# Optimization experiments

Hardware: AMD Instinct MI355X
Metric: run time of the kernel (lower is better)

## Reference

```python
import jax, jax.numpy as jnp
import numpy as np

H = 64      # hidden_dim
NH = 4      # attention heads
HD = H // NH
NC = 13     # num_classes
NF = 8      # node features


def setup_inputs() -> dict:
    key = jax.random.key(0)
    ks = iter(jax.random.split(key, 32))
    B, T, N, E = 4, 16, 4096, 32768
    s = 0.05
    d = {}
    d["node_features"] = jax.random.normal(next(ks), (B, T, N, NF), jnp.float32)
    d["edge_index"] = jax.random.randint(next(ks), (T, 2, E), 0, N, jnp.int32)
    # spatial conv (Linear(NF,H), ReLU, Linear(H,H))
    d["sc_w1"] = jax.random.normal(next(ks), (H, NF), jnp.float32) * s
    d["sc_b1"] = jnp.zeros((H,), jnp.float32)
    d["sc_w2"] = jax.random.normal(next(ks), (H, H), jnp.float32) * s
    d["sc_b2"] = jnp.zeros((H,), jnp.float32)
    # 2-layer LSTM (pytorch gate order i,f,g,o)
    for l in range(2):
        d[f"lstm_w_ih{l}"] = jax.random.normal(next(ks), (4 * H, H), jnp.float32) * s
        d[f"lstm_w_hh{l}"] = jax.random.normal(next(ks), (4 * H, H), jnp.float32) * s
        d[f"lstm_b_ih{l}"] = jnp.zeros((4 * H,), jnp.float32)
        d[f"lstm_b_hh{l}"] = jnp.zeros((4 * H,), jnp.float32)
    # MultiheadAttention in_proj / out_proj
    d["attn_w_in"] = jax.random.normal(next(ks), (3 * H, H), jnp.float32) * s
    d["attn_b_in"] = jnp.zeros((3 * H,), jnp.float32)
    d["attn_w_out"] = jax.random.normal(next(ks), (H, H), jnp.float32) * s
    d["attn_b_out"] = jnp.zeros((H,), jnp.float32)
    # predictor MLP (dropout inactive at eval)
    d["p_w1"] = jax.random.normal(next(ks), (2 * H, H), jnp.float32) * s
    d["p_b1"] = jnp.zeros((2 * H,), jnp.float32)
    d["p_w2"] = jax.random.normal(next(ks), (H, 2 * H), jnp.float32) * s
    d["p_b2"] = jnp.zeros((H,), jnp.float32)
    d["p_w3"] = jax.random.normal(next(ks), (NC, H), jnp.float32) * s
    d["p_b3"] = jnp.zeros((NC,), jnp.float32)
    return d


def _lstm_layer(x, w_ih, w_hh, b_ih, b_hh):
    # x: (T, BN, H_in) -> (T, BN, H)
    BN = x.shape[1]
    Hh = w_hh.shape[1]

    def step(carry, xt):
        h, c = carry
        z = xt @ w_ih.T + h @ w_hh.T + (b_ih + b_hh)
        i, f, g, o = jnp.split(z, 4, axis=-1)
        c = jax.nn.sigmoid(f) * c + jax.nn.sigmoid(i) * jnp.tanh(g)
        h = jax.nn.sigmoid(o) * jnp.tanh(c)
        return (h, c), h

    h0 = jnp.zeros((BN, Hh), x.dtype)
    _, ys = jax.lax.scan(step, (h0, h0), x)
    return ys


def _forward(node_features, edge_index, sc_w1, sc_b1, sc_w2, sc_b2,
             lstm_w_ih0, lstm_w_hh0, lstm_b_ih0, lstm_b_hh0,
             lstm_w_ih1, lstm_w_hh1, lstm_b_ih1, lstm_b_hh1,
             attn_w_in, attn_b_in, attn_w_out, attn_b_out,
             p_w1, p_b1, p_w2, p_b2, p_w3, p_b3):
    B, T, N, _ = node_features.shape
    # spatial conv applied to every (b,t,n)
    h = jax.nn.relu(jnp.einsum('btnf,hf->btnh', node_features, sc_w1) + sc_b1)
    h = jnp.einsum('btnh,gh->btng', h, sc_w2) + sc_b2  # (B,T,N,H)

    def agg_step(_, inp):
        h_t, edges = inp  # (B,N,H), (2,E)
        src, dst = edges[0], edges[1]
        msgs = h_t[:, src]  # (B,E,H) gathered from pre-update h_t (matches torch)
        ssum = jax.vmap(lambda m: jax.ops.segment_sum(m, dst, num_segments=N))(msgs)
        cnt = jax.ops.segment_sum(jnp.ones(dst.shape, h_t.dtype), dst, num_segments=N)
        mean = ssum / jnp.maximum(cnt, 1.0)[None, :, None]
        h_new = jnp.where(cnt[None, :, None] > 0, (h_t + mean) * 0.5, h_t)
        return None, h_new

    _, h_agg = jax.lax.scan(agg_step, None, (h.transpose(1, 0, 2, 3), edge_index))
    h = h_agg.transpose(1, 0, 2, 3)  # (B,T,N,H)

    # per-node temporal sequence: (T, B*N, H)
    x = h.transpose(0, 2, 1, 3).reshape(B * N, T, H).transpose(1, 0, 2)
    x = _lstm_layer(x, lstm_w_ih0, lstm_w_hh0, lstm_b_ih0, lstm_b_hh0)
    x = _lstm_layer(x, lstm_w_ih1, lstm_w_hh1, lstm_b_ih1, lstm_b_hh1)
    x = x.transpose(1, 0, 2)  # (BN,T,H)

    # multi-head self-attention (batch_first)
    qkv = x @ attn_w_in.T + attn_b_in
    q, k, v = jnp.split(qkv, 3, axis=-1)
    BN = q.shape[0]
    q = q.reshape(BN, T, NH, HD)
    k = k.reshape(BN, T, NH, HD)
    v = v.reshape(BN, T, NH, HD)
    scores = jnp.einsum('bthd,bshd->bhts', q, k) / jnp.sqrt(jnp.float32(HD)).astype(x.dtype)
    attn = jax.nn.softmax(scores, axis=-1)
    o = jnp.einsum('bhts,bshd->bthd', attn, v).reshape(BN, T, H)
    o = o @ attn_w_out.T + attn_b_out

    final = o[:, -1, :]  # (BN,H)
    z = jax.nn.relu(final @ p_w1.T + p_b1)
    z = jax.nn.relu(z @ p_w2.T + p_b2)
    logits = z @ p_w3.T + p_b3
    return logits.reshape(B, N, NC)


def reference(node_features, edge_index, sc_w1, sc_b1, sc_w2, sc_b2,
              lstm_w_ih0, lstm_w_hh0, lstm_b_ih0, lstm_b_hh0,
              lstm_w_ih1, lstm_w_hh1, lstm_b_ih1, lstm_b_hh1,
              attn_w_in, attn_b_in, attn_w_out, attn_b_out,
              p_w1, p_b1, p_w2, p_b2, p_w3, p_b3):
    return _forward(node_features, edge_index, sc_w1, sc_b1, sc_w2, sc_b2,
                    lstm_w_ih0, lstm_w_hh0, lstm_b_ih0, lstm_b_hh0,
                    lstm_w_ih1, lstm_w_hh1, lstm_b_ih1, lstm_b_hh1,
                    attn_w_in, attn_b_in, attn_w_out, attn_b_out,
                    p_w1, p_b1, p_w2, p_b2, p_w3, p_b3)
```

## Files before the change

kernel.cpp:

```cpp
#include <hip/hip_runtime.h>

constexpr int kB  = 4;
constexpr int kT  = 16;
constexpr int kN  = 4096;
constexpr int kBN = kB * kN;
constexpr int kE  = 32768;
constexpr int kNC = 13;

typedef _Float16 f16x8 __attribute__((ext_vector_type(8)));
typedef _Float16 f16x4 __attribute__((ext_vector_type(4)));
typedef float f32x4 __attribute__((ext_vector_type(4)));

__device__ __forceinline__ float sigm(float x) { return 1.f / (1.f + __expf(-x)); }
__device__ __forceinline__ float tanh_(float x) {
  float e = __expf(2.f * x);
  return 1.f - 2.f / (e + 1.f);
}

__device__ __forceinline__ void barrier_lds() {
  asm volatile("s_waitcnt lgkmcnt(0)\n\ts_barrier" ::: "memory");
}

__device__ __forceinline__ f32x4 mm3(f16x8 ah, f16x8 al, f16x8 bh, f16x8 bl, f32x4 acc) {
  acc = __builtin_amdgcn_mfma_f32_16x16x32_f16(ah, bh, acc, 0, 0, 0);
  acc = __builtin_amdgcn_mfma_f32_16x16x32_f16(ah, bl, acc, 0, 0, 0);
  acc = __builtin_amdgcn_mfma_f32_16x16x32_f16(al, bh, acc, 0, 0, 0);
  return acc;
}

__device__ __forceinline__ void split8(const float* p, f16x8& hi, f16x8& lo) {
  float4 u0 = *(const float4*)p, u1 = *(const float4*)(p + 4);
  float vv[8] = {u0.x, u0.y, u0.z, u0.w, u1.x, u1.y, u1.z, u1.w};
#pragma unroll
  for (int j = 0; j < 8; ++j) {
    _Float16 hj = (_Float16)vv[j];
    hi[j] = hj;
    lo[j] = (_Float16)(vv[j] - (float)hj);
  }
}

__device__ __forceinline__ void split8T(const float* base, int kbase, int seq,
                                        f16x8& hi, f16x8& lo) {
  float vv[8];
#pragma unroll
  for (int j = 0; j < 8; ++j) vv[j] = base[(kbase + j) * 68 + seq];
#pragma unroll
  for (int j = 0; j < 8; ++j) {
    _Float16 hj = (_Float16)vv[j];
    hi[j] = hj;
    lo[j] = (_Float16)(vv[j] - (float)hj);
  }
}

__device__ __forceinline__ unsigned int packf(float v) {
  _Float16 h = (_Float16)v;
  _Float16 l = (_Float16)(v - (float)h);
  unsigned short uh = __builtin_bit_cast(unsigned short, h);
  unsigned short ul = __builtin_bit_cast(unsigned short, l);
  return (unsigned int)uh | ((unsigned int)ul << 16);
}
__device__ __forceinline__ float up2(unsigned int w) {
  _Float16 h = __builtin_bit_cast(_Float16, (unsigned short)(w & 0xFFFFu));
  _Float16 l = __builtin_bit_cast(_Float16, (unsigned short)(w >> 16));
  return (float)h + (float)l;
}
__device__ __forceinline__ void unpack8(const unsigned int* w, f16x8& hi, f16x8& lo) {
#pragma unroll
  for (int j = 0; j < 8; ++j) {
    hi[j] = __builtin_bit_cast(_Float16, (unsigned short)(w[j] & 0xFFFFu));
    lo[j] = __builtin_bit_cast(_Float16, (unsigned short)(w[j] >> 16));
  }
}

__global__ __launch_bounds__(256, 2) void conv_kernel(
    const float* __restrict__ nf, const float* __restrict__ w1,
    const float* __restrict__ b1, const float* __restrict__ w2,
    const float* __restrict__ b2, unsigned int* __restrict__ hpk) {
  __shared__ unsigned int act[256 * 68];
  int tid = threadIdx.x;
  int w = tid >> 6, lane = tid & 63;
  int q = lane >> 4, i = lane & 15;
  int flat0 = blockIdx.x * 256;
  int bb = flat0 >> 16;
  int t = (flat0 >> 12) & 15;
  int n0 = flat0 & 4095;

  f16x8 w1h[4], w1l[4];
  f16x8 w2h[4][2], w2l[4][2];
  float bias1[4], bias2[4];
#pragma unroll
  for (int nt = 0; nt < 4; ++nt) {
    int n = nt * 16 + i;
    if (q == 0) split8(w1 + n * 8, w1h[nt], w1l[nt]);
    else { w1h[nt] = (f16x8)0; w1l[nt] = (f16x8)0; }
#pragma unroll
    for (int ks = 0; ks < 2; ++ks)
      split8(w2 + n * 64 + ks * 32 + q * 8, w2h[nt][ks], w2l[nt][ks]);
    bias1[nt] = b1[n];
    bias2[nt] = b2[n];
  }

  f16x8 xh[4], xl[4];
#pragma unroll
  for (int Mt = 0; Mt < 4; ++Mt) {
    if (q == 0)
      split8(nf + (size_t)(flat0 + w * 64 + Mt * 16 + i) * 8, xh[Mt], xl[Mt]);
    else { xh[Mt] = (f16x8)0; xl[Mt] = (f16x8)0; }
  }
#pragma unroll
  for (int Mt = 0; Mt < 4; ++Mt)
#pragma unroll
    for (int nt = 0; nt < 4; ++nt) {
      f32x4 acc = {bias1[nt], bias1[nt], bias1[nt], bias1[nt]};
      acc = mm3(xh[Mt], xl[Mt], w1h[nt], w1l[nt], acc);
#pragma unroll
      for (int r = 0; r < 4; ++r)
        act[(w * 64 + Mt * 16 + q * 4 + r) * 68 + nt * 16 + i] =
            packf(fmaxf(acc[r], 0.f));
    }
  __syncthreads();

  f32x4 acc2[4][4];
#pragma unroll
  for (int Mt = 0; Mt < 4; ++Mt)
#pragma unroll
    for (int nt = 0; nt < 4; ++nt) {
      acc2[Mt][nt][0] = bias2[nt]; acc2[Mt][nt][1] = bias2[nt];
      acc2[Mt][nt][2] = bias2[nt]; acc2[Mt][nt][3] = bias2[nt];
    }
#pragma unroll
  for (int ks = 0; ks < 2; ++ks)
#pragma unroll
    for (int Mt = 0; Mt < 4; ++Mt) {
      const unsigned int* p = &act[(w * 64 + Mt * 16 + i) * 68 + ks * 32 + q * 8];
      unsigned int wd[8];
#pragma unroll
      for (int j = 0; j < 4; ++j) {
        uint2 u = *(const uint2*)(p + j * 2);
        wd[2 * j] = u.x; wd[2 * j + 1] = u.y;
      }
      f16x8 ah, al;
      unpack8(wd, ah, al);
#pragma unroll
      for (int nt = 0; nt < 4; ++nt)
        acc2[Mt][nt] = mm3(ah, al, w2h[nt][ks], w2l[nt][ks], acc2[Mt][nt]);
    }
  __syncthreads();
#pragma unroll
  for (int Mt = 0; Mt < 4; ++Mt)
#pragma unroll
    for (int nt = 0; nt < 4; ++nt)
#pragma unroll
      for (int r = 0; r < 4; ++r)
        act[(w * 64 + Mt * 16 + q * 4 + r) * 68 + nt * 16 + i] =
            packf(acc2[Mt][nt][r]);
  __syncthreads();
  size_t tbase = ((size_t)t * kBN + (size_t)bb * kN + n0) * 64;
#pragma unroll
  for (int k = 0; k < 16; ++k) {
    int d0 = (k * 256 + tid) * 4;
    int node = d0 >> 6, ch = d0 & 63;
    uint2 a = *(const uint2*)&act[node * 68 + ch];
    uint2 b = *(const uint2*)&act[node * 68 + ch + 2];
    uint4 vv = {a.x, a.y, b.x, b.y};
    *(uint4*)(hpk + tbase + d0) = vv;
  }
}

__global__ __launch_bounds__(256) void count_kernel(
    const int* __restrict__ ei, int* __restrict__ cnt) {
  int i = blockIdx.x * 256 + threadIdx.x;
  int t = i >> 15, e = i & (kE - 1);
  int dst = ei[t * 2 * kE + kE + e];
  atomicAdd(&cnt[t * kN + dst], 1);
}

__global__ __launch_bounds__(1024) void scan_kernel(
    const int* __restrict__ cnt, int* __restrict__ off, int* __restrict__ cur) {
  __shared__ int sdata[1024];
  int t = blockIdx.x;
  int tid = threadIdx.x;
  const int* c = cnt + t * kN;
  int v0 = c[tid * 4], v1 = c[tid * 4 + 1], v2 = c[tid * 4 + 2], v3 = c[tid * 4 + 3];
  int s = v0 + v1 + v2 + v3;
  sdata[tid] = s;
  __syncthreads();
  for (int d = 1; d < 1024; d <<= 1) {
    int add = (tid >= d) ? sdata[tid - d] : 0;
    __syncthreads();
    sdata[tid] += add;
    __syncthreads();
  }
  int base = sdata[tid] - s;
  int o = t * kN + tid * 4;
  off[o] = base;            cur[o] = base;
  off[o + 1] = base + v0;   cur[o + 1] = base + v0;
  off[o + 2] = base + v0 + v1;        cur[o + 2] = base + v0 + v1;
  off[o + 3] = base + v0 + v1 + v2;   cur[o + 3] = base + v0 + v1 + v2;
}

__global__ __launch_bounds__(256) void place_kernel(
    const int* __restrict__ ei, int* __restrict__ cur, int* __restrict__ csr) {
  int i = blockIdx.x * 256 + threadIdx.x;
  int t = i >> 15, e = i & (kE - 1);
  int src = ei[t * 2 * kE + e];
  int dst = ei[t * 2 * kE + kE + e];
  int pos = atomicAdd(&cur[t * kN + dst], 1);
  csr[t * kE + pos] = src;
}

__global__ __launch_bounds__(256) void gather_kernel(
    const unsigned int* __restrict__ hpk, const int* __restrict__ csr,
    const int* __restrict__ off, const int* __restrict__ cnt,
    _Float16* __restrict__ xhi, _Float16* __restrict__ xlo) {
  int blk = blockIdx.x;
  int t = (blk & 7) | ((blk >> 13) << 3);
  int idx = (blk >> 3) & 1023;
  int d = idx * 4 + (threadIdx.x >> 6);
  int lane = threadIdx.x & 63;
  int b = lane >> 4, cq = lane & 15;
  int o = off[t * kN + d];
  int c = cnt[t * kN + d];
  size_t tb = ((size_t)t * kBN + (size_t)b * kN) * 64 + cq * 4;
  const int* cs = csr + t * kE + o;
  float s[4] = {0.f, 0.f, 0.f, 0.f};
  int j = 0;
  for (; j + 4 <= c; j += 4) {
    int i0 = cs[j], i1 = cs[j + 1], i2 = cs[j + 2], i3 = cs[j + 3];
    uint4 v0 = *(const uint4*)(hpk + tb + (size_t)i0 * 64);
    uint4 v1 = *(const uint4*)(hpk + tb + (size_t)i1 * 64);
    uint4 v2 = *(const uint4*)(hpk + tb + (size_t)i2 * 64);
    uint4 v3 = *(const uint4*)(hpk + tb + (size_t)i3 * 64);
    s[0] += up2(v0.x) + up2(v1.x) + up2(v2.x) + up2(v3.x);
    s[1] += up2(v0.y) + up2(v1.y) + up2(v2.y) + up2(v3.y);
    s[2] += up2(v0.z) + up2(v1.z) + up2(v2.z) + up2(v3.z);
    s[3] += up2(v0.w) + up2(v1.w) + up2(v2.w) + up2(v3.w);
  }
  for (; j < c; ++j) {
    int i0 = cs[j];
    uint4 v0 = *(const uint4*)(hpk + tb + (size_t)i0 * 64);
    s[0] += up2(v0.x); s[1] += up2(v0.y); s[2] += up2(v0.z); s[3] += up2(v0.w);
  }
  uint4 hv = *(const uint4*)(hpk + tb + (size_t)d * 64);
  float hvf[4] = {up2(hv.x), up2(hv.y), up2(hv.z), up2(hv.w)};
  f16x4 ohi, olo;
  float inv = (c > 0) ? 1.f / (float)c : 0.f;
#pragma unroll
  for (int u = 0; u < 4; ++u) {
    float ov = (c > 0) ? (hvf[u] + s[u] * inv) * 0.5f : hvf[u];
    _Float16 hi = (_Float16)ov;
    ohi[u] = hi;
    olo[u] = (_Float16)(ov - (float)hi);
  }
  *(f16x4*)(xhi + tb + (size_t)d * 64) = ohi;
  *(f16x4*)(xlo + tb + (size_t)d * 64) = olo;
}

__global__ __launch_bounds__(512, 2) void lstm2_kernel(
    const _Float16* __restrict__ xhi, const _Float16* __restrict__ xlo,
    _Float16* __restrict__ yhi, _Float16* __restrict__ ylo,
    const float* __restrict__ wih0, const float* __restrict__ whh0,
    const float* __restrict__ bih0, const float* __restrict__ bhh0,
    const float* __restrict__ wih1, const float* __restrict__ whh1,
    const float* __restrict__ bih1, const float* __restrict__ bhh1) {
  __shared__ _Float16 h1f[2][4][2][2][512];
  __shared__ _Float16 h2f[2][4][2][2][512];
  int tid = threadIdx.x;
  int grp = tid >> 8;
  int cb = (tid >> 6) & 3, lane = tid & 63;
  int q = lane >> 4, i = lane & 15;
  int s0 = blockIdx.x * 64;

  const float* Wih = grp ? wih1 : wih0;
  const float* Whh = grp ? whh1 : whh0;
  const float* Bih = grp ? bih1 : bih0;
  const float* Bhh = grp ? bhh1 : bhh0;

  f16x8 wr[2][4][2][2];
#pragma unroll
  for (int mat = 0; mat < 2; ++mat) {
    const float* W = mat ? Whh : Wih;
#pragma unroll
    for (int g = 0; g < 4; ++g) {
      int row = (g * 4 + cb) * 16 + i;
#pragma unroll
      for (int ks = 0; ks < 2; ++ks)
        split8(W + row * 64 + ks * 32 + q * 8, wr[mat][g][ks][0], wr[mat][g][ks][1]);
    }
  }
  int ch = cb * 16 + i;
  float bias4[4];
#pragma unroll
  for (int g = 0; g < 4; ++g) bias4[g] = Bih[g * 64 + ch] + Bhh[g * 64 + ch];
  float cst[4][4];
#pragma unroll
  for (int Mt = 0; Mt < 4; ++Mt)
#pragma unroll
    for (int r = 0; r < 4; ++r) cst[Mt][r] = 0.f;
  int ks2 = ch >> 5, q2 = (ch >> 3) & 3, j2 = ch & 7;
  int p = 0;

  for (int it = 0; it < kT + 1; ++it) {
    if (grp == 0) {
      if (it < kT) {
        int t = it;
#pragma unroll
        for (int mp = 0; mp < 2; ++mp) {
          f32x4 acc[2][4];
#pragma unroll
          for (int ml = 0; ml < 2; ++ml)
#pragma unroll
            for (int g = 0; g < 4; ++g) {
              acc[ml][g][0] = bias4[g]; acc[ml][g][1] = bias4[g];
              acc[ml][g][2] = bias4[g]; acc[ml][g][3] = bias4[g];
            }
#pragma unroll
          for (int ks = 0; ks < 2; ++ks) {
            f16x8 xah[2], xal[2];
#pragma unroll
            for (int ml = 0; ml < 2; ++ml) {
              size_t base = ((size_t)t * kBN + s0 + (2 * mp + ml) * 16 + i) * 64 + ks * 32 + q * 8;
              xah[ml] = *(const f16x8*)(xhi + base);
              xal[ml] = *(const f16x8*)(xlo + base);
            }
#pragma unroll
            for (int g = 0; g < 4; ++g)
#pragma unroll
              for (int ml = 0; ml < 2; ++ml)
                acc[ml][g] = mm3(xah[ml], xal[ml], wr[0][g][ks][0], wr[0][g][ks][1], acc[ml][g]);
          }
          if (t > 0) {
#pragma unroll
            for (int ks = 0; ks < 2; ++ks) {
              f16x8 hah[2], hal[2];
#pragma unroll
              for (int ml = 0; ml < 2; ++ml) {
                hah[ml] = *(const f16x8*)&h1f[p][2 * mp + ml][ks][0][lane * 8];
                hal[ml] = *(const f16x8*)&h1f[p][2 * mp + ml][ks][1][lane * 8];
              }
#pragma unroll
              for (int g = 0; g < 4; ++g)
#pragma unroll
                for (int ml = 0; ml < 2; ++ml)
                  acc[ml][g] = mm3(hah[ml], hal[ml], wr[1][g][ks][0], wr[1][g][ks][1], acc[ml][g]);
            }
          }
#pragma unroll
          for (int ml = 0; ml < 2; ++ml) {
            int Mt = 2 * mp + ml;
#pragma unroll
            for (int r = 0; r < 4; ++r) {
              float zi = acc[ml][0][r], zf = acc[ml][1][r];
              float zg = acc[ml][2][r], zo = acc[ml][3][r];
              float ig = sigm(zi), fg = sigm(zf), gg = tanh_(zg), og = sigm(zo);
              float c = fg * cst[Mt][r] + ig * gg;
              cst[Mt][r] = c;
              float hv = og * tanh_(c);
              int row = q * 4 + r;
              _Float16 hh = (_Float16)hv;
              _Float16 hl = (_Float16)(hv - (float)hh);
              int lane2 = q2 * 16 + row;
              h1f[p ^ 1][Mt][ks2][0][lane2 * 8 + j2] = hh;
              h1f[p ^ 1][Mt][ks2][1][lane2 * 8 + j2] = hl;
            }
          }
        }
      }
    } else {
      if (it >= 1) {
        int t = it - 1;
#pragma unroll
        for (int mp = 0; mp < 2; ++mp) {
          f32x4 acc[2][4];
#pragma unroll
          for (int ml = 0; ml < 2; ++ml)
#pragma unroll
            for (int g = 0; g < 4; ++g) {
              acc[ml][g][0] = bias4[g]; acc[ml][g][1] = bias4[g];
              acc[ml][g][2] = bias4[g]; acc[ml][g][3] = bias4[g];
            }
#pragma unroll
          for (int ks = 0; ks < 2; ++ks) {
            f16x8 xah[2], xal[2];
#pragma unroll
            for (int ml = 0; ml < 2; ++ml) {
              xah[ml] = *(const f16x8*)&h1f[p][2 * mp + ml][ks][0][lane * 8];
              xal[ml] = *(const f16x8*)&h1f[p][2 * mp + ml][ks][1][lane * 8];
            }
#pragma unroll
            for (int g = 0; g < 4; ++g)
#pragma unroll
              for (int ml = 0; ml < 2; ++ml)
                acc[ml][g] = mm3(xah[ml], xal[ml], wr[0][g][ks][0], wr[0][g][ks][1], acc[ml][g]);
          }
          if (t > 0) {
#pragma unroll
            for (int ks = 0; ks < 2; ++ks) {
              f16x8 hah[2], hal[2];
#pragma unroll
              for (int ml = 0; ml < 2; ++ml) {
                hah[ml] = *(const f16x8*)&h2f[p][2 * mp + ml][ks][0][lane * 8];
                hal[ml] = *(const f16x8*)&h2f[p][2 * mp + ml][ks][1][lane * 8];
              }
#pragma unroll
              for (int g = 0; g < 4; ++g)
#pragma unroll
                for (int ml = 0; ml < 2; ++ml)
                  acc[ml][g] = mm3(hah[ml], hal[ml], wr[1][g][ks][0], wr[1][g][ks][1], acc[ml][g]);
            }
          }
#pragma unroll
          for (int ml = 0; ml < 2; ++ml) {
            int Mt = 2 * mp + ml;
#pragma unroll
            for (int r = 0; r < 4; ++r) {
              float zi = acc[ml][0][r], zf = acc[ml][1][r];
              float zg = acc[ml][2][r], zo = acc[ml][3][r];
              float ig = sigm(zi), fg = sigm(zf), gg = tanh_(zg), og = sigm(zo);
              float c = fg * cst[Mt][r] + ig * gg;
              cst[Mt][r] = c;
              float hv = og * tanh_(c);
              int row = q * 4 + r;
              size_t ob = ((size_t)t * kBN + s0 + Mt * 16 + row) * 64 + ch;
              _Float16 hh = (_Float16)hv;
              _Float16 hl = (_Float16)(hv - (float)hh);
              yhi[ob] = hh;
              ylo[ob] = hl;
              int lane2 = q2 * 16 + row;
              h2f[p ^ 1][Mt][ks2][0][lane2 * 8 + j2] = hh;
              h2f[p ^ 1][Mt][ks2][1][lane2 * 8 + j2] = hl;
            }
          }
        }
      }
    }
    barrier_lds();
    p ^= 1;
  }
}

__device__ __forceinline__ void stage_frags64(const float* W, _Float16* base,
                                              int O, int tid) {
  int total = O * 16;
  for (int idx = tid; idx < total; idx += 256) {
    int r = idx >> 4, k4 = idx & 15;
    float4 v = *(const float4*)&W[r * 64 + k4 * 4];
    int k = k4 * 4;
    int nt = r >> 4, ii = r & 15, ks = k >> 5, qq = (k >> 3) & 3, j0 = k & 7;
    _Float16* dh = base + ((nt * 2 + ks) * 2) * 512 + (qq * 16 + ii) * 8 + j0;
    _Float16* dl = dh + 512;
    float vv[4] = {v.x, v.y, v.z, v.w};
#pragma unroll
    for (int u = 0; u < 4; ++u) {
      _Float16 hh = (_Float16)vv[u];
      dh[u] = hh;
      dl[u] = (_Float16)(vv[u] - (float)hh);
    }
  }
}

__device__ __forceinline__ void stage_frags128(const float* W, _Float16* base,
                                               int O, int tid) {
  int total = O * 32;
  for (int idx = tid; idx < total; idx += 256) {
    int r = idx >> 5, k4 = idx & 31;
    float4 v = *(const float4*)&W[r * 128 + k4 * 4];
    int k = k4 * 4;
    int nt = r >> 4, ii = r & 15, ks = k >> 5, qq = (k >> 3) & 3, j0 = k & 7;
    _Float16* dh = base + ((nt * 4 + ks) * 2) * 512 + (qq * 16 + ii) * 8 + j0;
    _Float16* dl = dh + 512;
    float vv[4] = {v.x, v.y, v.z, v.w};
#pragma unroll
    for (int u = 0; u < 4; ++u) {
      _Float16 hh = (_Float16)vv[u];
      dh[u] = hh;
      dl[u] = (_Float16)(vv[u] - (float)hh);
    }
  }
}

__global__ __launch_bounds__(256, 1) void head_kernel(
    const _Float16* __restrict__ xhi, const _Float16* __restrict__ xlo,
    const float* __restrict__ win, const float* __restrict__ bin,
    const float* __restrict__ wout, const float* __restrict__ bout,
    const float* __restrict__ pw1, const float* __restrict__ pb1,
    const float* __restrict__ pw2, const float* __restrict__ pb2,
    const float* __restrict__ pw3, const float* __restrict__ pb3,
    float* __restrict__ out) {
  __shared__ __align__(16) float smem[30720];
  _Float16* wb = (_Float16*)smem;
  float* buf = smem + 21504;

  int tid = threadIdx.x;
  int w = tid >> 6, lane = tid & 63;
  int q = lane >> 4, i = lane & 15;
  int s0 = blockIdx.x * 64;

  stage_frags64(win, wb, 64, tid);
  stage_frags64(win + 64 * 64, wb + 8192, 128, tid);
  __syncthreads();

  {
    f16x8 ah[2], al[2];
#pragma unroll
    for (int ks = 0; ks < 2; ++ks) {
      size_t base = ((size_t)15 * kBN + s0 + w * 16 + i) * 64 + ks * 32 + q * 8;
      ah[ks] = *(const f16x8*)(xhi + base);
      al[ks] = *(const f16x8*)(xlo + base);
    }
#pragma unroll
    for (int nt = 0; nt < 4; ++nt) {
      float bias = bin[nt * 16 + i];
      f32x4 acc = {bias, bias, bias, bias};
#pragma unroll
      for (int ks = 0; ks < 2; ++ks) {
        const _Float16* bp = wb + ((nt * 2 + ks) * 2) * 512 + lane * 8;
        acc = mm3(ah[ks], al[ks], *(const f16x8*)bp, *(const f16x8*)(bp + 512), acc);
      }
      *(float4*)&buf[(nt * 16 + i) * 68 + w * 16 + q * 4] = *(float4*)&acc;
    }
  }
  __syncthreads();
  float qreg[16];
#pragma unroll
  for (int d = 0; d < 16; ++d) qreg[d] = buf[(w * 16 + d) * 68 + lane];
  __syncthreads();

  float m = -1e30f, l = 0.f;
  float o[16];
#pragma unroll
  for (int d = 0; d < 16; ++d) o[d] = 0.f;

  for (int t = 0; t < kT; ++t) {
    f16x8 xah[4][2], xal[4][2];
#pragma unroll
    for (int Mt = 0; Mt < 4; ++Mt)
#pragma unroll
      for (int ks = 0; ks < 2; ++ks) {
        size_t base = ((size_t)t * kBN + s0 + Mt * 16 + i) * 64 + ks * 32 + q * 8;
        xah[Mt][ks] = *(const f16x8*)(xhi + base);
        xal[Mt][ks] = *(const f16x8*)(xlo + base);
      }
#pragma unroll
    for (int u = 0; u < 2; ++u) {
      int nt = 2 * w + u;
      float bias = bin[64 + nt * 16 + i];
      f16x8 bh[2], bl[2];
#pragma unroll
      for (int ks = 0; ks < 2; ++ks) {
        const _Float16* bp = wb + 8192 + ((nt * 2 + ks) * 2) * 512 + lane * 8;
        bh[ks] = *(const f16x8*)bp;
        bl[ks] = *(const f16x8*)(bp + 512);
      }
#pragma unroll
      for (int Mt = 0; Mt < 4; ++Mt) {
        f32x4 acc = {bias, bias, bias, bias};
#pragma unroll
        for (int ks = 0; ks < 2; ++ks)
          acc = mm3(xah[Mt][ks], xal[Mt][ks], bh[ks], bl[ks], acc);
        *(float4*)&buf[(nt * 16 + i) * 68 + Mt * 16 + q * 4] = *(float4*)&acc;
      }
    }
    __syncthreads();
    float sc = 0.f;
#pragma unroll
    for (int d = 0; d < 16; ++d) sc += qreg[d] * buf[(w * 16 + d) * 68 + lane];
    sc *= 0.25f;
    float mn = fmaxf(m, sc);
    float alpha = __expf(m - mn);
    float pp = __expf(sc - mn);
    l = l * alpha + pp;
#pragma unroll
    for (int d = 0; d < 16; ++d)
      o[d] = o[d] * alpha + pp * buf[(64 + w * 16 + d) * 68 + lane];
    m = mn;
    __syncthreads();
  }

  float linv = 1.f / l;
#pragma unroll
  for (int d = 0; d < 16; ++d) buf[(w * 16 + d) * 68 + lane] = o[d] * linv;
  __syncthreads();

  stage_frags64(wout, wb, 64, tid);
  stage_frags64(pw1, wb + 8192, 128, tid);
  stage_frags128(pw2, wb + 24576, 64, tid);
  for (int idx = tid; idx < 256; idx += 256) {
    int r = idx >> 4, k4 = idx & 15;
    float4 v = {0.f, 0.f, 0.f, 0.f};
    if (r < kNC) v = *(const float4*)&pw3[r * 64 + k4 * 4];
    int k = k4 * 4;
    int ks = k >> 5, qq = (k >> 3) & 3, j0 = k & 7;
    _Float16* dh = wb + 40960 + (ks * 2) * 512 + (qq * 16 + r) * 8 + j0;
    _Float16* dl = dh + 512;
    float vv[4] = {v.x, v.y, v.z, v.w};
#pragma unroll
    for (int u = 0; u < 4; ++u) {
      _Float16 hh = (_Float16)vv[u];
      dh[u] = hh;
      dl[u] = (_Float16)(vv[u] - (float)hh);
    }
  }
  __syncthreads();

  int seq = w * 16 + i;

  {
    f16x8 ah[2], al[2];
    split8T(buf, q * 8, seq, ah[0], al[0]);
    split8T(buf, 32 + q * 8, seq, ah[1], al[1]);
#pragma unroll
    for (int nt = 0; nt < 4; ++nt) {
      float bias = bout[nt * 16 + i];
      f32x4 acc = {bias, bias, bias, bias};
#pragma unroll
      for (int ks = 0; ks < 2; ++ks) {
        const _Float16* bp = wb + ((nt * 2 + ks) * 2) * 512 + lane * 8;
        acc = mm3(ah[ks], al[ks], *(const f16x8*)bp, *(const f16x8*)(bp + 512), acc);
      }
      *(float4*)&buf[4352 + (nt * 16 + i) * 68 + w * 16 + q * 4] = *(float4*)&acc;
    }
  }
  __syncthreads();

  {
    f16x8 ah[2], al[2];
    split8T(buf + 4352, q * 8, seq, ah[0], al[0]);
    split8T(buf + 4352, 32 + q * 8, seq, ah[1], al[1]);
    __syncthreads();
#pragma unroll
    for (int nt = 0; nt < 8; ++nt) {
      float bias = pb1[nt * 16 + i];
      f32x4 acc = {bias, bias, bias, bias};
#pragma unroll
      for (int ks = 0; ks < 2; ++ks) {
        const _Float16* bp = wb + 8192 + ((nt * 2 + ks) * 2) * 512 + lane * 8;
        acc = mm3(ah[ks], al[ks], *(const f16x8*)bp, *(const f16x8*)(bp + 512), acc);
      }
      f32x4 r4;
#pragma unroll
      for (int r = 0; r < 4; ++r) r4[r] = fmaxf(acc[r], 0.f);
      *(float4*)&buf[(nt * 16 + i) * 68 + w * 16 + q * 4] = *(float4*)&r4;
    }
  }
  __syncthreads();

  {
    f16x8 ah[4], al[4];
#pragma unroll
    for (int ks = 0; ks < 4; ++ks)
      split8T(buf, ks * 32 + q * 8, seq, ah[ks], al[ks]);
    __syncthreads();
#pragma unroll
    for (int nt = 0; nt < 4; ++nt) {
      float bias = pb2[nt * 16 + i];
      f32x4 acc = {bias, bias, bias, bias};
#pragma unroll
      for (int ks = 0; ks < 4; ++ks) {
        const _Float16* bp = wb + 24576 + ((nt * 4 + ks) * 2) * 512 + lane * 8;
        acc = mm3(ah[ks], al[ks], *(const f16x8*)bp, *(const f16x8*)(bp + 512), acc);
      }
      f32x4 r4;
#pragma unroll
      for (int r = 0; r < 4; ++r) r4[r] = fmaxf(acc[r], 0.f);
      *(float4*)&buf[(nt * 16 + i) * 68 + w * 16 + q * 4] = *(float4*)&r4;
    }
  }
  __syncthreads();

  {
    f16x8 ah[2], al[2];
    split8T(buf, q * 8, seq, ah[0], al[0]);
    split8T(buf, 32 + q * 8, seq, ah[1], al[1]);
    f32x4 acc = {0.f, 0.f, 0.f, 0.f};
#pragma unroll
    for (int ks = 0; ks < 2; ++ks) {
      const _Float16* bp = wb + 40960 + (ks * 2) * 512 + lane * 8;
      acc = mm3(ah[ks], al[ks], *(const f16x8*)bp, *(const f16x8*)(bp + 512), acc);
    }
    if (i < kNC) {
      float bb = pb3[i];
#pragma unroll
      for (int r = 0; r < 4; ++r)
        out[(size_t)(s0 + w * 16 + q * 4 + r) * kNC + i] = acc[r] + bb;
    }
  }
}

extern "C" void kernel_launch(void* const* d_in, const int* in_sizes, int n_in,
                              void* d_out, int out_size, void* d_ws, size_t ws_size,
                              hipStream_t stream) {
  const float* nf    = (const float*)d_in[0];
  const int*   ei    = (const int*)d_in[1];
  const float* sc_w1 = (const float*)d_in[2];
  const float* sc_b1 = (const float*)d_in[3];
  const float* sc_w2 = (const float*)d_in[4];
  const float* sc_b2 = (const float*)d_in[5];
  const float* wih0  = (const float*)d_in[6];
  const float* whh0  = (const float*)d_in[7];
  const float* bih0  = (const float*)d_in[8];
  const float* bhh0  = (const float*)d_in[9];
  const float* wih1  = (const float*)d_in[10];
  const float* whh1  = (const float*)d_in[11];
  const float* bih1  = (const float*)d_in[12];
  const float* bhh1  = (const float*)d_in[13];
  const float* win   = (const float*)d_in[14];
  const float* bin   = (const float*)d_in[15];
  const float* wout  = (const float*)d_in[16];
  const float* bout  = (const float*)d_in[17];
  const float* pw1   = (const float*)d_in[18];
  const float* pb1   = (const float*)d_in[19];
  const float* pw2   = (const float*)d_in[20];
  const float* pb2   = (const float*)d_in[21];
  const float* pw3   = (const float*)d_in[22];
  const float* pb3   = (const float*)d_in[23];
  float* out = (float*)d_out;

  const size_t NB = (size_t)kT * kBN * 64;
  unsigned int* Hpk = (unsigned int*)d_ws;
  _Float16* Ahi = (_Float16*)(Hpk + NB);
  _Float16* Alo = Ahi + NB;
  _Float16* Bhi = Alo + NB;
  _Float16* Blo = Bhi + NB;
  int* cnt = (int*)(Blo + NB);
  int* off = cnt + kT * kN;
  int* cur = off + kT * kN;
  int* csr = cur + kT * kN;

  hipMemsetAsync(cnt, 0, (size_t)kT * kN * sizeof(int), stream);

  conv_kernel<<<1024, 256, 0, stream>>>(nf, sc_w1, sc_b1, sc_w2, sc_b2, Hpk);
  count_kernel<<<2048, 256, 0, stream>>>(ei, cnt);
  scan_kernel<<<16, 1024, 0, stream>>>(cnt, off, cur);
  place_kernel<<<2048, 256, 0, stream>>>(ei, cur, csr);
  gather_kernel<<<16384, 256, 0, stream>>>(Hpk, csr, off, cnt, Bhi, Blo);
  lstm2_kernel<<<256, 512, 0, stream>>>(Bhi, Blo, Ahi, Alo,
                                        wih0, whh0, bih0, bhh0,
                                        wih1, whh1, bih1, bhh1);
  head_kernel<<<256, 256, 0, stream>>>(Ahi, Alo, win, bin, wout, bout,
                                       pw1, pb1, pw2, pb2, pw3, pb3, out);
}
```

Measured before the change: 419.3 us.

## Pack LSTM output hi/lo into one buffer and drop head weight LDS staging

The LSTM kernel now writes its hi/lo fp16 split output as packed 32-bit words into a single buffer instead of two separate fp16 arrays. The head kernel reads these packed words and no longer stages weights into a large shared-memory fragment buffer. Instead each wave loads and splits weight fragments straight from global memory into registers, with the K/V weights held in registers across the time loop. This shrinks LDS use so occupancy can rise (launch bounds raised to 3 blocks), and removes the staging passes and their barriers. The cost is redundant global weight loads and register pressure. The per-element scattered 4-byte stores in the LSTM may also change write efficiency.

```diff
diff --git a/kernel.cpp b/kernel.cpp
--- a/kernel.cpp
+++ b/kernel.cpp
@@ -59,6 +59,11 @@
   unsigned short ul = __builtin_bit_cast(unsigned short, l);
   return (unsigned int)uh | ((unsigned int)ul << 16);
 }
+__device__ __forceinline__ unsigned int pack2(_Float16 h, _Float16 l) {
+  unsigned short uh = __builtin_bit_cast(unsigned short, h);
+  unsigned short ul = __builtin_bit_cast(unsigned short, l);
+  return (unsigned int)uh | ((unsigned int)ul << 16);
+}
 __device__ __forceinline__ float up2(unsigned int w) {
   _Float16 h = __builtin_bit_cast(_Float16, (unsigned short)(w & 0xFFFFu));
   _Float16 l = __builtin_bit_cast(_Float16, (unsigned short)(w >> 16));
@@ -70,6 +75,12 @@
     hi[j] = __builtin_bit_cast(_Float16, (unsigned short)(w[j] & 0xFFFFu));
     lo[j] = __builtin_bit_cast(_Float16, (unsigned short)(w[j] >> 16));
   }
+}
+__device__ __forceinline__ void loadpk8(const unsigned int* p, f16x8& hi, f16x8& lo) {
+  uint4 u0 = *(const uint4*)p;
+  uint4 u1 = *(const uint4*)(p + 4);
+  unsigned int wd[8] = {u0.x, u0.y, u0.z, u0.w, u1.x, u1.y, u1.z, u1.w};
+  unpack8(wd, hi, lo);
 }
 
 __global__ __launch_bounds__(256, 2) void conv_kernel(
@@ -258,7 +269,7 @@
 
 __global__ __launch_bounds__(512, 2) void lstm2_kernel(
     const _Float16* __restrict__ xhi, const _Float16* __restrict__ xlo,
-    _Float16* __restrict__ yhi, _Float16* __restrict__ ylo,
+    unsigned int* __restrict__ ypk,
     const float* __restrict__ wih0, const float* __restrict__ whh0,
     const float* __restrict__ bih0, const float* __restrict__ bhh0,
     const float* __restrict__ wih1, const float* __restrict__ whh1,
@@ -424,8 +435,7 @@
               size_t ob = ((size_t)t * kBN + s0 + Mt * 16 + row) * 64 + ch;
               _Float16 hh = (_Float16)hv;
               _Float16 hl = (_Float16)(hv - (float)hh);
-              yhi[ob] = hh;
-              ylo[ob] = hl;
+              ypk[ob] = pack2(hh, hl);
               int lane2 = q2 * 16 + row;
               h2f[p ^ 1][Mt][ks2][0][lane2 * 8 + j2] = hh;
               h2f[p ^ 1][Mt][ks2][1][lane2 * 8 + j2] = hl;
@@ -439,84 +449,48 @@
   }
 }
 
-__device__ __forceinline__ void stage_frags64(const float* W, _Float16* base,
-                                              int O, int tid) {
-  int total = O * 16;
-  for (int idx = tid; idx < total; idx += 256) {
-    int r = idx >> 4, k4 = idx & 15;
-    float4 v = *(const float4*)&W[r * 64 + k4 * 4];
-    int k = k4 * 4;
-    int nt = r >> 4, ii = r & 15, ks = k >> 5, qq = (k >> 3) & 3, j0 = k & 7;
-    _Float16* dh = base + ((nt * 2 + ks) * 2) * 512 + (qq * 16 + ii) * 8 + j0;
-    _Float16* dl = dh + 512;
-    float vv[4] = {v.x, v.y, v.z, v.w};
-#pragma unroll
-    for (int u = 0; u < 4; ++u) {
-      _Float16 hh = (_Float16)vv[u];
-      dh[u] = hh;
-      dl[u] = (_Float16)(vv[u] - (float)hh);
-    }
-  }
-}
-
-__device__ __forceinline__ void stage_frags128(const float* W, _Float16* base,
-                                               int O, int tid) {
-  int total = O * 32;
-  for (int idx = tid; idx < total; idx += 256) {
-    int r = idx >> 5, k4 = idx & 31;
-    float4 v = *(const float4*)&W[r * 128 + k4 * 4];
-    int k = k4 * 4;
-    int nt = r >> 4, ii = r & 15, ks = k >> 5, qq = (k >> 3) & 3, j0 = k & 7;
-    _Float16* dh = base + ((nt * 4 + ks) * 2) * 512 + (qq * 16 + ii) * 8 + j0;
-    _Float16* dl = dh + 512;
-    float vv[4] = {v.x, v.y, v.z, v.w};
-#pragma unroll
-    for (int u = 0; u < 4; ++u) {
-      _Float16 hh = (_Float16)vv[u];
-      dh[u] = hh;
-      dl[u] = (_Float16)(vv[u] - (float)hh);
-    }
-  }
-}
-
-__global__ __launch_bounds__(256, 1) void head_kernel(
-    const _Float16* __restrict__ xhi, const _Float16* __restrict__ xlo,
+__global__ __launch_bounds__(256, 3) void head_kernel(
+    const unsigned int* __restrict__ ypk,
     const float* __restrict__ win, const float* __restrict__ bin,
     const float* __restrict__ wout, const float* __restrict__ bout,
     const float* __restrict__ pw1, const float* __restrict__ pb1,
     const float* __restrict__ pw2, const float* __restrict__ pb2,
     const float* __restrict__ pw3, const float* __restrict__ pb3,
     float* __restrict__ out) {
-  __shared__ __align__(16) float smem[30720];
-  _Float16* wb = (_Float16*)smem;
-  float* buf = smem + 21504;
+  __shared__ __align__(16) float buf[8704];
 
   int tid = threadIdx.x;
   int w = tid >> 6, lane = tid & 63;
   int q = lane >> 4, i = lane & 15;
   int s0 = blockIdx.x * 64;
 
-  stage_frags64(win, wb, 64, tid);
-  stage_frags64(win + 64 * 64, wb + 8192, 128, tid);
-  __syncthreads();
+  f16x8 kvh[2][2], kvl[2][2];
+#pragma unroll
+  for (int u = 0; u < 2; ++u) {
+    int nt = 2 * w + u;
+#pragma unroll
+    for (int ks = 0; ks < 2; ++ks)
+      split8(win + (size_t)(64 + nt * 16 + i) * 64 + ks * 32 + q * 8,
+             kvh[u][ks], kvl[u][ks]);
+  }
 
   {
     f16x8 ah[2], al[2];
 #pragma unroll
-    for (int ks = 0; ks < 2; ++ks) {
-      size_t base = ((size_t)15 * kBN + s0 + w * 16 + i) * 64 + ks * 32 + q * 8;
-      ah[ks] = *(const f16x8*)(xhi + base);
-      al[ks] = *(const f16x8*)(xlo + base);
-    }
+    for (int ks = 0; ks < 2; ++ks)
+      loadpk8(ypk + ((size_t)15 * kBN + s0 + w * 16 + i) * 64 + ks * 32 + q * 8,
+              ah[ks], al[ks]);
 #pragma unroll
     for (int nt = 0; nt < 4; ++nt) {
+      f16x8 bh[2], bl[2];
+#pragma unroll
+      for (int ks = 0; ks < 2; ++ks)
+        split8(win + (size_t)(nt * 16 + i) * 64 + ks * 32 + q * 8, bh[ks], bl[ks]);
       float bias = bin[nt * 16 + i];
       f32x4 acc = {bias, bias, bias, bias};
 #pragma unroll
-      for (int ks = 0; ks < 2; ++ks) {
-        const _Float16* bp = wb + ((nt * 2 + ks) * 2) * 512 + lane * 8;
-        acc = mm3(ah[ks], al[ks], *(const f16x8*)bp, *(const f16x8*)(bp + 512), acc);
-      }
+      for (int ks = 0; ks < 2; ++ks)
+        acc = mm3(ah[ks], al[ks], bh[ks], bl[ks], acc);
       *(float4*)&buf[(nt * 16 + i) * 68 + w * 16 + q * 4] = *(float4*)&acc;
     }
   }
@@ -532,33 +506,27 @@
   for (int d = 0; d < 16; ++d) o[d] = 0.f;
 
   for (int t = 0; t < kT; ++t) {
-    f16x8 xah[4][2], xal[4][2];
-#pragma unroll
-    for (int Mt = 0; Mt < 4; ++Mt)
-#pragma unroll
-      for (int ks = 0; ks < 2; ++ks) {
-        size_t base = ((size_t)t * kBN + s0 + Mt * 16 + i) * 64 + ks * 32 + q * 8;
-        xah[Mt][ks] = *(const f16x8*)(xhi + base);
-        xal[Mt][ks] = *(const f16x8*)(xlo + base);
-      }
-#pragma unroll
-    for (int u = 0; u < 2; ++u) {
-      int nt = 2 * w + u;
-      float bias = bin[64 + nt * 16 + i];
-      f16x8 bh[2], bl[2];
-#pragma unroll
-      for (int ks = 0; ks < 2; ++ks) {
-        const _Float16* bp = wb + 8192 + ((nt * 2 + ks) * 2) * 512 + lane * 8;
-        bh[ks] = *(const f16x8*)bp;
-        bl[ks] = *(const f16x8*)(bp + 512);
-      }
-#pragma unroll
-      for (int Mt = 0; Mt < 4; ++Mt) {
-        f32x4 acc = {bias, bias, bias, bias};
+#pragma unroll
+    for (int mp = 0; mp < 2; ++mp) {
+      f16x8 xah[2][2], xal[2][2];
+#pragma unroll
+      for (int ml = 0; ml < 2; ++ml)
 #pragma unroll
         for (int ks = 0; ks < 2; ++ks)
-          acc = mm3(xah[Mt][ks], xal[Mt][ks], bh[ks], bl[ks], acc);
-        *(float4*)&buf[(nt * 16 + i) * 68 + Mt * 16 + q * 4] = *(float4*)&acc;
+          loadpk8(ypk + ((size_t)t * kBN + s0 + (2 * mp + ml) * 16 + i) * 64 + ks * 32 + q * 8,
+                  xah[ml][ks], xal[ml][ks]);
+#pragma unroll
+      for (int u = 0; u < 2; ++u) {
+        int nt = 2 * w + u;
+        float bias = bin[64 + nt * 16 + i];
+#pragma unroll
+        for (int ml = 0; ml < 2; ++ml) {
+          f32x4 acc = {bias, bias, bias, bias};
+#pragma unroll
+          for (int ks = 0; ks < 2; ++ks)
+            acc = mm3(xah[ml][ks], xal[ml][ks], kvh[u][ks], kvl[u][ks], acc);
+          *(float4*)&buf[(nt * 16 + i) * 68 + (2 * mp + ml) * 16 + q * 4] = *(float4*)&acc;
+        }
       }
     }
     __syncthreads();
@@ -582,27 +550,6 @@
   for (int d = 0; d < 16; ++d) buf[(w * 16 + d) * 68 + lane] = o[d] * linv;
   __syncthreads();
 
-  stage_frags64(wout, wb, 64, tid);
-  stage_frags64(pw1, wb + 8192, 128, tid);
-  stage_frags128(pw2, wb + 24576, 64, tid);
-  for (int idx = tid; idx < 256; idx += 256) {
-    int r = idx >> 4, k4 = idx & 15;
-    float4 v = {0.f, 0.f, 0.f, 0.f};
-    if (r < kNC) v = *(const float4*)&pw3[r * 64 + k4 * 4];
-    int k = k4 * 4;
-    int ks = k >> 5, qq = (k >> 3) & 3, j0 = k & 7;
-    _Float16* dh = wb + 40960 + (ks * 2) * 512 + (qq * 16 + r) * 8 + j0;
-    _Float16* dl = dh + 512;
-    float vv[4] = {v.x, v.y, v.z, v.w};
-#pragma unroll
-    for (int u = 0; u < 4; ++u) {
-      _Float16 hh = (_Float16)vv[u];
-      dh[u] = hh;
-      dl[u] = (_Float16)(vv[u] - (float)hh);
-    }
-  }
-  __syncthreads();
-
   int seq = w * 16 + i;
 
   {
@@ -611,13 +558,15 @@
     split8T(buf, 32 + q * 8, seq, ah[1], al[1]);
 #pragma unroll
     for (int nt = 0; nt < 4; ++nt) {
+      f16x8 bh[2], bl[2];
+#pragma unroll
+      for (int ks = 0; ks < 2; ++ks)
+        split8(wout + (size_t)(nt * 16 + i) * 64 + ks * 32 + q * 8, bh[ks], bl[ks]);
       float bias = bout[nt * 16 + i];
       f32x4 acc = {bias, bias, bias, bias};
 #pragma unroll
-      for (int ks = 0; ks < 2; ++ks) {
-        const _Float16* bp = wb + ((nt * 2 + ks) * 2) * 512 + lane * 8;
-        acc = mm3(ah[ks], al[ks], *(const f16x8*)bp, *(const f16x8*)(bp + 512), acc);
-      }
+      for (int ks = 0; ks < 2; ++ks)
+        acc = mm3(ah[ks], al[ks], bh[ks], bl[ks], acc);
       *(float4*)&buf[4352 + (nt * 16 + i) * 68 + w * 16 + q * 4] = *(float4*)&acc;
     }
   }
@@ -630,13 +579,15 @@
     __syncthreads();
 #pragma unroll
     for (int nt = 0; nt < 8; ++nt) {
+      f16x8 bh[2], bl[2];
+#pragma unroll
+      for (int ks = 0; ks < 2; ++ks)
+        split8(pw1 + (size_t)(nt * 16 + i) * 64 + ks * 32 + q * 8, bh[ks], bl[ks]);
       float bias = pb1[nt * 16 + i];
       f32x4 acc = {bias, bias, bias, bias};
 #pragma unroll
-      for (int ks = 0; ks < 2; ++ks) {
-        const _Float16* bp = wb + 8192 + ((nt * 2 + ks) * 2) * 512 + lane * 8;
-        acc = mm3(ah[ks], al[ks], *(const f16x8*)bp, *(const f16x8*)(bp + 512), acc);
-      }
+      for (int ks = 0; ks < 2; ++ks)
+        acc = mm3(ah[ks], al[ks], bh[ks], bl[ks], acc);
       f32x4 r4;
 #pragma unroll
       for (int r = 0; r < 4; ++r) r4[r] = fmaxf(acc[r], 0.f);
@@ -657,8 +608,9 @@
       f32x4 acc = {bias, bias, bias, bias};
 #pragma unroll
       for (int ks = 0; ks < 4; ++ks) {
-        const _Float16* bp = wb + 24576 + ((nt * 4 + ks) * 2) * 512 + lane * 8;
-        acc = mm3(ah[ks], al[ks], *(const f16x8*)bp, *(const f16x8*)(bp + 512), acc);
+        f16x8 bh, bl;
+        split8(pw2 + (size_t)(nt * 16 + i) * 128 + ks * 32 + q * 8, bh, bl);
+        acc = mm3(ah[ks], al[ks], bh, bl, acc);
       }
       f32x4 r4;
 #pragma unroll
@@ -672,12 +624,19 @@
     f16x8 ah[2], al[2];
     split8T(buf, q * 8, seq, ah[0], al[0]);
     split8T(buf, 32 + q * 8, seq, ah[1], al[1]);
+    f16x8 bh[2], bl[2];
+#pragma unroll
+    for (int ks = 0; ks < 2; ++ks) {
+      if (i < kNC) {
+        split8(pw3 + (size_t)i * 64 + ks * 32 + q * 8, bh[ks], bl[ks]);
+      } else {
+        bh[ks] = (f16x8)0; bl[ks] = (f16x8)0;
+      }
+    }
     f32x4 acc = {0.f, 0.f, 0.f, 0.f};
 #pragma unroll
-    for (int ks = 0; ks < 2; ++ks) {
-      const _Float16* bp = wb + 40960 + (ks * 2) * 512 + lane * 8;
-      acc = mm3(ah[ks], al[ks], *(const f16x8*)bp, *(const f16x8*)(bp + 512), acc);
-    }
+    for (int ks = 0; ks < 2; ++ks)
+      acc = mm3(ah[ks], al[ks], bh[ks], bl[ks], acc);
     if (i < kNC) {
       float bb = pb3[i];
 #pragma unroll
@@ -718,11 +677,10 @@
 
   const size_t NB = (size_t)kT * kBN * 64;
   unsigned int* Hpk = (unsigned int*)d_ws;
-  _Float16* Ahi = (_Float16*)(Hpk + NB);
-  _Float16* Alo = Ahi + NB;
-  _Float16* Bhi = Alo + NB;
+  _Float16* Bhi = (_Float16*)(Hpk + NB);
   _Float16* Blo = Bhi + NB;
-  int* cnt = (int*)(Blo + NB);
+  unsigned int* Ypk = (unsigned int*)(Blo + NB);
+  int* cnt = (int*)(Ypk + NB);
   int* off = cnt + kT * kN;
   int* cur = off + kT * kN;
   int* csr = cur + kT * kN;
@@ -734,9 +692,9 @@
   scan_kernel<<<16, 1024, 0, stream>>>(cnt, off, cur);
   place_kernel<<<2048, 256, 0, stream>>>(ei, cur, csr);
   gather_kernel<<<16384, 256, 0, stream>>>(Hpk, csr, off, cnt, Bhi, Blo);
-  lstm2_kernel<<<256, 512, 0, stream>>>(Bhi, Blo, Ahi, Alo,
+  lstm2_kernel<<<256, 512, 0, stream>>>(Bhi, Blo, Ypk,
                                         wih0, whh0, bih0, bhh0,
                                         wih1, whh1, bih1, bhh1);
-  head_kernel<<<256, 256, 0, stream>>>(Ahi, Alo, win, bin, wout, bout,
+  head_kernel<<<256, 256, 0, stream>>>(Ypk, win, bin, wout, bout,
                                        pw1, pb1, pw2, pb2, pw3, pb3, out);
 }
```

Result: no change. 424.5 us (+1.2%).
